# Optimization experiments

Measured on AMD Instinct MI355X. Metric: run time of the kernel, lower is better.

The kernel has to match this reference:

```python
import jax, jax.numpy as jnp
import numpy as np

DIM = 1024
DEPTH = 8
DIM_HEAD = 64
HEADS = 16
NUM_Q = 16
EMB = 768
OUT = 1024
FF_INNER = 4 * DIM
INNER = DIM_HEAD * HEADS  # 1024
B, N1 = 64, 577
EPS = 1e-5


def _ln(x, g, b):
    mu = jnp.mean(x, axis=-1, keepdims=True)
    var = jnp.mean((x - mu) ** 2, axis=-1, keepdims=True)
    return (x - mu) * jax.lax.rsqrt(var + EPS) * g + b


def setup_inputs() -> dict:
    key = jax.random.key(0)
    ks = jax.random.split(key, 16)
    std = 0.02
    inp = {
        'x': jax.random.normal(ks[0], (B, N1, EMB), jnp.float32),
        'queries': jax.random.normal(ks[1], (1, NUM_Q, DIM), jnp.float32) / DIM ** 0.5,
        'proj_in_w': jax.random.normal(ks[2], (EMB, DIM), jnp.float32) * std,
        'proj_in_b': jnp.zeros((DIM,), jnp.float32),
        'ln1_g': jnp.ones((DEPTH, DIM), jnp.float32),
        'ln1_b': jnp.zeros((DEPTH, DIM), jnp.float32),
        'ln2_g': jnp.ones((DEPTH, DIM), jnp.float32),
        'ln2_b': jnp.zeros((DEPTH, DIM), jnp.float32),
        'wq': jax.random.normal(ks[3], (DEPTH, DIM, INNER), jnp.float32) * std,
        'wkv': jax.random.normal(ks[4], (DEPTH, DIM, 2 * INNER), jnp.float32) * std,
        'wo': jax.random.normal(ks[5], (DEPTH, INNER, DIM), jnp.float32) * std,
        'ffln_g': jnp.ones((DEPTH, DIM), jnp.float32),
        'ffln_b': jnp.zeros((DEPTH, DIM), jnp.float32),
        'w1': jax.random.normal(ks[6], (DEPTH, DIM, FF_INNER), jnp.float32) * std,
        'w2': jax.random.normal(ks[7], (DEPTH, FF_INNER, DIM), jnp.float32) * std,
        'proj_out_w': jax.random.normal(ks[8], (DIM, OUT), jnp.float32) * std,
        'proj_out_b': jnp.zeros((OUT,), jnp.float32),
        'nout_g': jnp.ones((OUT,), jnp.float32),
        'nout_b': jnp.zeros((OUT,), jnp.float32),
    }
    return inp


def reference(x, queries, proj_in_w, proj_in_b, ln1_g, ln1_b, ln2_g, ln2_b,
              wq, wkv, wo, ffln_g, ffln_b, w1, w2,
              proj_out_w, proj_out_b, nout_g, nout_b):
    b = x.shape[0]
    xp = x @ proj_in_w + proj_in_b          # (b, n1, dim)
    latents0 = jnp.broadcast_to(queries, (b, NUM_Q, DIM))
    scale = DIM_HEAD ** -0.25               # applied to both q and k

    def layer(latents, p):
        (g1, b1, g2, b2, Wq, Wkv, Wo, gf, bf, W1, W2) = p
        xn = _ln(xp, g1, b1)                # (b, n1, dim)
        lt = _ln(latents, g2, b2)           # (b, nq, dim)
        q = lt @ Wq                         # (b, nq, inner)
        kv_in = jnp.concatenate([xn, lt], axis=1)   # (b, n1+nq, dim)
        kv = kv_in @ Wkv                    # (b, n1+nq, 2*inner)
        k, v = jnp.split(kv, 2, axis=-1)
        L = kv_in.shape[1]
        qh = q.reshape(b, NUM_Q, HEADS, DIM_HEAD).transpose(0, 2, 1, 3)
        kh = k.reshape(b, L, HEADS, DIM_HEAD).transpose(0, 2, 1, 3)
        vh = v.reshape(b, L, HEADS, DIM_HEAD).transpose(0, 2, 1, 3)
        logits = jnp.einsum('bhqd,bhkd->bhqk', qh * scale, kh * scale)
        w = jax.nn.softmax(logits.astype(jnp.float32), axis=-1).astype(logits.dtype)
        o = jnp.einsum('bhqk,bhkd->bhqd', w, vh)
        o = o.transpose(0, 2, 1, 3).reshape(b, NUM_Q, INNER) @ Wo
        latents = o + latents
        h = _ln(latents, gf, bf) @ W1
        h = jax.nn.gelu(h, approximate=False)
        latents = h @ W2 + latents
        return latents, None

    params = (ln1_g, ln1_b, ln2_g, ln2_b, wq, wkv, wo, ffln_g, ffln_b, w1, w2)
    latents, _ = jax.lax.scan(layer, latents0, params)
    out = latents @ proj_out_w + proj_out_b
    return _ln(out, nout_g, nout_b)
```

## Files before the change

kernel.cpp:

```cpp
#include <hip/hip_runtime.h>
#include <hip/hip_bf16.h>
#include <math.h>

#define DEV __device__ __forceinline__

typedef __bf16 bf16x8 __attribute__((ext_vector_type(8)));
typedef float f32x4 __attribute__((ext_vector_type(4)));
typedef unsigned short u16x8 __attribute__((ext_vector_type(8)));
typedef unsigned short u16x4 __attribute__((ext_vector_type(4)));

DEV float b2f(unsigned short u){ unsigned int i = ((unsigned int)u)<<16; float f; __builtin_memcpy(&f,&i,4); return f; }
DEV unsigned short f2b(float x){ unsigned int i; __builtin_memcpy(&i,&x,4); unsigned int r = i + 0x7FFFu + ((i>>16)&1u); return (unsigned short)(r>>16); }

DEV int swz(int row, int elem){ return row*64 + ((((elem>>3) ^ row) & 7)<<3) + (elem&7); }

enum { EPI_F32=0, EPI_GELU=2, EPI_RESF32=3 };

template<int BM, int BN>
__global__ __launch_bounds__(256)
void gemm_lds(const unsigned short* __restrict__ A, const unsigned short* __restrict__ Bt,
              const float* __restrict__ bias, unsigned short* __restrict__ Out,
              int M, int N, int K, int NT)
{
    constexpr int MR = BM/32, NR = BN/32;
    constexpr int SA = BM/8, SB = BN/8;
    __shared__ unsigned short As[BM*64];
    __shared__ unsigned short Bs[BN*64];
    const int tid  = threadIdx.x;
    const int lane = tid & 63;
    const int wave = tid >> 6;
    const int wr = wave >> 1, wc = wave & 1;
    const int chunk = gridDim.x >> 3;
    const int nb = (blockIdx.x & 7)*chunk + (blockIdx.x >> 3);
    const int nt = nb % NT, mt = nb / NT;
    const int lr = lane >> 3;
    const int lc = lane & 7;

    f32x4 acc[MR][NR];
    #pragma unroll
    for (int m=0;m<MR;m++)
      #pragma unroll
      for (int n=0;n<NR;n++) acc[m][n] = f32x4{0.f,0.f,0.f,0.f};

    auto stage = [&](int k0){
      #pragma unroll
      for (int i=0;i<SA/4;i++){
        int s = wave*(SA/4) + i;
        int row = s*8 + lr;
        const unsigned short* src = A + (size_t)(mt*BM+row)*K + k0 + (((lc ^ row)&7)<<3);
        __builtin_amdgcn_global_load_lds((const unsigned int*)src, (unsigned int*)&As[s*512], 16, 0, 0);
      }
      #pragma unroll
      for (int i=0;i<SB/4;i++){
        int s = wave*(SB/4) + i;
        int row = s*8 + lr;
        const unsigned short* src = Bt + (size_t)(nt*BN+row)*K + k0 + (((lc ^ row)&7)<<3);
        __builtin_amdgcn_global_load_lds((const unsigned int*)src, (unsigned int*)&Bs[s*512], 16, 0, 0);
      }
    };

    const int nk = K / 64;
    #pragma unroll 1
    for (int kt=0; kt<nk; kt++){
      stage(kt*64);
      __syncthreads();
      #pragma unroll
      for (int kk=0; kk<2; kk++){
        bf16x8 av[MR], bv[NR];
        #pragma unroll
        for (int m=0;m<MR;m++){
          int r = wr*(BM/2) + m*16 + (lane&15);
          av[m] = (bf16x8)(*reinterpret_cast<const u16x8*>(&As[swz(r, kk*32 + (lane>>4)*8)]));
        }
        #pragma unroll
        for (int n=0;n<NR;n++){
          int r = wc*(BN/2) + n*16 + (lane&15);
          bv[n] = (bf16x8)(*reinterpret_cast<const u16x8*>(&Bs[swz(r, kk*32 + (lane>>4)*8)]));
        }
        #pragma unroll
        for (int m=0;m<MR;m++)
          #pragma unroll
          for (int n=0;n<NR;n++)
            acc[m][n] = __builtin_amdgcn_mfma_f32_16x16x32_bf16(av[m], bv[n], acc[m][n], 0, 0, 0);
      }
      __syncthreads();
    }

    #pragma unroll
    for (int m=0;m<MR;m++){
      #pragma unroll
      for (int n=0;n<NR;n++){
        #pragma unroll
        for (int r=0;r<4;r++){
          int row = mt*BM + wr*(BM/2) + m*16 + (lane>>4)*4 + r;
          int col = nt*BN + wc*(BN/2) + n*16 + (lane&15);
          if (row < M){
            float v = acc[m][n][r];
            if (bias) v += bias[col];
            Out[(size_t)row*N + col] = f2b(v);
          }
        }
      }
    }
}

template<int EPI>
__global__ __launch_bounds__(256)
void gemm_sp(const unsigned short* __restrict__ AH, const unsigned short* __restrict__ AL,
             const unsigned short* __restrict__ BH, const unsigned short* __restrict__ BL,
             const float* __restrict__ bias, const float* __restrict__ Res,
             void* __restrict__ Out, unsigned short* __restrict__ OutL,
             int M, int N, int K, int NT)
{
    constexpr int MR=2, NR=2;
    __shared__ unsigned short As[2*64*64];
    __shared__ unsigned short Bs[2*64*64];
    const int tid  = threadIdx.x;
    const int lane = tid & 63;
    const int wave = tid >> 6;
    const int wr = wave >> 1, wc = wave & 1;
    const int chunk = gridDim.x >> 3;
    const int nb = (blockIdx.x & 7)*chunk + (blockIdx.x >> 3);
    const int nt = nb % NT, mt = nb / NT;
    const int lr = lane >> 3;
    const int lc = lane & 7;

    f32x4 acc[MR][NR];
    #pragma unroll
    for (int m=0;m<MR;m++)
      #pragma unroll
      for (int n=0;n<NR;n++) acc[m][n] = f32x4{0.f,0.f,0.f,0.f};

    auto stage = [&](int k0){
      #pragma unroll
      for (int i=0;i<2;i++){
        int s = wave*2 + i;
        int row = s*8 + lr;
        int scol = ((lc ^ row)&7)<<3;
        size_t aofs = (size_t)(mt*64+row)*K + k0 + scol;
        size_t bofs = (size_t)(nt*64+row)*K + k0 + scol;
        __builtin_amdgcn_global_load_lds((const unsigned int*)(AH+aofs), (unsigned int*)&As[s*512],        16, 0, 0);
        __builtin_amdgcn_global_load_lds((const unsigned int*)(AL+aofs), (unsigned int*)&As[4096 + s*512], 16, 0, 0);
        __builtin_amdgcn_global_load_lds((const unsigned int*)(BH+bofs), (unsigned int*)&Bs[s*512],        16, 0, 0);
        __builtin_amdgcn_global_load_lds((const unsigned int*)(BL+bofs), (unsigned int*)&Bs[4096 + s*512], 16, 0, 0);
      }
    };

    const int nk = K / 64;
    #pragma unroll 1
    for (int kt=0; kt<nk; kt++){
      stage(kt*64);
      __syncthreads();
      #pragma unroll
      for (int kk=0; kk<2; kk++){
        bf16x8 ah[MR], al[MR], bh[NR], bl[NR];
        #pragma unroll
        for (int m=0;m<MR;m++){
          int a = swz(wr*32 + m*16 + (lane&15), kk*32 + (lane>>4)*8);
          ah[m] = (bf16x8)(*reinterpret_cast<const u16x8*>(&As[a]));
          al[m] = (bf16x8)(*reinterpret_cast<const u16x8*>(&As[4096 + a]));
        }
        #pragma unroll
        for (int n=0;n<NR;n++){
          int a = swz(wc*32 + n*16 + (lane&15), kk*32 + (lane>>4)*8);
          bh[n] = (bf16x8)(*reinterpret_cast<const u16x8*>(&Bs[a]));
          bl[n] = (bf16x8)(*reinterpret_cast<const u16x8*>(&Bs[4096 + a]));
        }
        #pragma unroll
        for (int m=0;m<MR;m++)
          #pragma unroll
          for (int n=0;n<NR;n++){
            acc[m][n] = __builtin_amdgcn_mfma_f32_16x16x32_bf16(ah[m], bh[n], acc[m][n], 0, 0, 0);
            acc[m][n] = __builtin_amdgcn_mfma_f32_16x16x32_bf16(ah[m], bl[n], acc[m][n], 0, 0, 0);
            acc[m][n] = __builtin_amdgcn_mfma_f32_16x16x32_bf16(al[m], bh[n], acc[m][n], 0, 0, 0);
          }
      }
      __syncthreads();
    }

    #pragma unroll
    for (int m=0;m<MR;m++){
      #pragma unroll
      for (int n=0;n<NR;n++){
        #pragma unroll
        for (int r=0;r<4;r++){
          int row = mt*64 + wr*32 + m*16 + (lane>>4)*4 + r;
          int col = nt*64 + wc*32 + n*16 + (lane&15);
          float v = acc[m][n][r];
          if (bias) v += bias[col];
          if constexpr (EPI==EPI_GELU){
            v = 0.5f*v*(1.0f + erff(v*0.70710678118654752f));
            unsigned short hi = f2b(v);
            ((unsigned short*)Out)[(size_t)row*N + col] = hi;
            OutL[(size_t)row*N + col] = f2b(v - b2f(hi));
          } else {
            if constexpr (EPI==EPI_RESF32) v += Res[(size_t)row*N + col];
            ((float*)Out)[(size_t)row*N + col] = v;
          }
        }
      }
    }
}

enum { OM_F32=0, OM_BF16=1, OM_SPLIT=2 };
template<bool INF32, int OM, bool HASGB>
__global__ __launch_bounds__(256)
void ln_rows(const void* __restrict__ In, void* __restrict__ Out,
             unsigned short* __restrict__ OutL,
             const float* __restrict__ g, const float* __restrict__ bb)
{
  const int row = blockIdx.x;
  const int tid = threadIdx.x;
  const size_t base = (size_t)row*1024 + tid*4;
  float v[4];
  if constexpr (INF32){
    f32x4 t = *reinterpret_cast<const f32x4*>((const float*)In + base);
    v[0]=t[0]; v[1]=t[1]; v[2]=t[2]; v[3]=t[3];
  } else {
    u16x4 t = *reinterpret_cast<const u16x4*>((const unsigned short*)In + base);
    #pragma unroll
    for (int j=0;j<4;j++) v[j] = b2f(t[j]);
  }
  float s = v[0]+v[1]+v[2]+v[3];
  float q = v[0]*v[0]+v[1]*v[1]+v[2]*v[2]+v[3]*v[3];
  #pragma unroll
  for (int o=32;o>0;o>>=1){ s += __shfl_xor(s,o,64); q += __shfl_xor(q,o,64); }
  __shared__ float sm[8];
  const int wave = tid>>6, lane = tid&63;
  if (lane==0){ sm[wave] = s; sm[4+wave] = q; }
  __syncthreads();
  s = sm[0]+sm[1]+sm[2]+sm[3];
  q = sm[4]+sm[5]+sm[6]+sm[7];
  const float mean = s*(1.f/1024.f);
  const float rstd = rsqrtf(fmaxf(q*(1.f/1024.f) - mean*mean, 0.f) + 1e-5f);
  #pragma unroll
  for (int j=0;j<4;j++){
    float t2 = (v[j]-mean)*rstd;
    if constexpr (HASGB) t2 = t2*g[tid*4+j] + bb[tid*4+j];
    v[j] = t2;
  }
  if constexpr (OM==OM_F32){
    f32x4 t{v[0],v[1],v[2],v[3]};
    *reinterpret_cast<f32x4*>((float*)Out + base) = t;
  } else if constexpr (OM==OM_BF16){
    u16x4 t{f2b(v[0]),f2b(v[1]),f2b(v[2]),f2b(v[3])};
    *reinterpret_cast<u16x4*>((unsigned short*)Out + base) = t;
  } else {
    u16x4 h{f2b(v[0]),f2b(v[1]),f2b(v[2]),f2b(v[3])};
    u16x4 l{f2b(v[0]-b2f(h[0])),f2b(v[1]-b2f(h[1])),f2b(v[2]-b2f(h[2])),f2b(v[3]-b2f(h[3]))};
    *reinterpret_cast<u16x4*>((unsigned short*)Out + base) = h;
    *reinterpret_cast<u16x4*>(OutL + base) = l;
  }
}

template<bool LO>
__global__ __launch_bounds__(256)
void transpose_cvt(const float* __restrict__ W, const float* __restrict__ rs,
                   unsigned short* __restrict__ Wt, unsigned short* __restrict__ Wtlo,
                   int K, int N)
{
  __shared__ float t[32][33];
  const int tx = threadIdx.x & 31, ty = threadIdx.x >> 5;
  const int n0 = blockIdx.x*32, k0 = blockIdx.y*32;
  #pragma unroll
  for (int j=0;j<4;j++){
    int r = ty + j*8;
    float w = W[(size_t)(k0+r)*N + n0 + tx];
    if (rs) w *= rs[k0+r];
    t[r][tx] = w;
  }
  __syncthreads();
  #pragma unroll
  for (int j=0;j<4;j++){
    int r = ty + j*8;
    float w = t[tx][r];
    unsigned short hi = f2b(w);
    Wt[(size_t)(n0+r)*K + k0 + tx] = hi;
    if constexpr (LO)
      Wtlo[(size_t)(n0+r)*K + k0 + tx] = f2b(w - b2f(hi));
  }
}

__global__ __launch_bounds__(256)
void biaskv_kernel(const float* __restrict__ ln1b, const float* __restrict__ wkv,
                   float* __restrict__ out)
{
  const int l = blockIdx.y;
  const int n = blockIdx.x*256 + threadIdx.x;
  const float* b1 = ln1b + l*1024;
  const float* W  = wkv + (size_t)l*1024*2048;
  float s = 0.f;
  for (int k=0;k<1024;k++) s += b1[k]*W[(size_t)k*2048 + n];
  out[l*2048 + n] = s;
}

__global__ __launch_bounds__(256)
void init_latents(const float* __restrict__ Q, float* __restrict__ L)
{
  size_t idx = ((size_t)blockIdx.x*256 + threadIdx.x)*4;
  int row = (int)(idx >> 10);
  int col = (int)(idx & 1023);
  f32x4 t = *reinterpret_cast<const f32x4*>(Q + (size_t)(row & 15)*1024 + col);
  *reinterpret_cast<f32x4*>(L + idx) = t;
}

__global__ __launch_bounds__(256)
void cvt_f32_bf16(const float* __restrict__ In, unsigned short* __restrict__ Out, size_t n4)
{
  size_t i = (size_t)blockIdx.x*256 + threadIdx.x;
  if (i >= n4) return;
  f32x4 t = *reinterpret_cast<const f32x4*>(In + i*4);
  u16x4 u{f2b(t[0]),f2b(t[1]),f2b(t[2]),f2b(t[3])};
  *reinterpret_cast<u16x4*>(Out + i*4) = u;
}

__global__ __launch_bounds__(256)
void cvt_f32b_pair(const float* __restrict__ In, unsigned short* __restrict__ Oh,
                   unsigned short* __restrict__ Ol)
{
  size_t idx = ((size_t)blockIdx.x*256 + threadIdx.x)*4;
  f32x4 t = *reinterpret_cast<const f32x4*>(In + idx);
  u16x4 h{f2b(t[0]),f2b(t[1]),f2b(t[2]),f2b(t[3])};
  u16x4 l{f2b(t[0]-b2f(h[0])),f2b(t[1]-b2f(h[1])),f2b(t[2]-b2f(h[2])),f2b(t[3]-b2f(h[3]))};
  *reinterpret_cast<u16x4*>(Oh + idx) = h;
  *reinterpret_cast<u16x4*>(Ol + idx) = l;
}

__global__ __launch_bounds__(256)
void attn_kernel(const float* __restrict__ QLTf,
                 const unsigned short* __restrict__ KVX,
                 const float* __restrict__ KVLTf,
                 unsigned short* __restrict__ ATTOh,
                 unsigned short* __restrict__ ATTOl)
{
  __shared__ float qs[16][64];
  __shared__ float ws[16][600];
  const int tid = threadIdx.x;
  const int bh = blockIdx.x;
  const int b = bh >> 4, h = bh & 15;

  {
    int idx = tid*4;
    int qi = idx >> 6, d = idx & 63;
    f32x4 t = *reinterpret_cast<const f32x4*>(QLTf + (size_t)(b*16+qi)*1024 + h*64 + d);
    #pragma unroll
    for (int j=0;j<4;j++) qs[qi][d+j] = 0.125f * t[j];
  }
  __syncthreads();

  for (int r = tid; r < 593; r += 256){
    float a[16];
    #pragma unroll
    for (int qi=0;qi<16;qi++) a[qi] = 0.f;
    if (r < 577){
      const unsigned short* krow = KVX + ((size_t)(b*577 + r)*2048 + h*64);
      #pragma unroll 4
      for (int d4=0; d4<16; d4++){
        u16x4 k4 = *reinterpret_cast<const u16x4*>(krow + d4*4);
        float kf0=b2f(k4[0]), kf1=b2f(k4[1]), kf2=b2f(k4[2]), kf3=b2f(k4[3]);
        #pragma unroll
        for (int qi=0;qi<16;qi++){
          f32x4 q4 = *reinterpret_cast<const f32x4*>(&qs[qi][d4*4]);
          a[qi] += q4[0]*kf0 + q4[1]*kf1 + q4[2]*kf2 + q4[3]*kf3;
        }
      }
    } else {
      const float* krow = KVLTf + ((size_t)(b*16 + (r-577))*2048 + h*64);
      #pragma unroll 4
      for (int d4=0; d4<16; d4++){
        f32x4 k4 = *reinterpret_cast<const f32x4*>(krow + d4*4);
        #pragma unroll
        for (int qi=0;qi<16;qi++){
          f32x4 q4 = *reinterpret_cast<const f32x4*>(&qs[qi][d4*4]);
          a[qi] += q4[0]*k4[0] + q4[1]*k4[1] + q4[2]*k4[2] + q4[3]*k4[3];
        }
      }
    }
    #pragma unroll
    for (int qi=0;qi<16;qi++) ws[qi][r] = a[qi];
  }
  __syncthreads();

  const int wave = tid>>6, lane = tid&63;
  for (int qi = wave; qi < 16; qi += 4){
    float m = -1e30f;
    for (int r = lane; r < 593; r += 64) m = fmaxf(m, ws[qi][r]);
    #pragma unroll
    for (int o=32;o>0;o>>=1) m = fmaxf(m, __shfl_xor(m,o,64));
    float s = 0.f;
    for (int r = lane; r < 593; r += 64){ float e = expf(ws[qi][r]-m); ws[qi][r] = e; s += e; }
    #pragma unroll
    for (int o=32;o>0;o>>=1) s += __shfl_xor(s,o,64);
    float inv = 1.f/s;
    for (int r = lane; r < 593; r += 64) ws[qi][r] *= inv;
  }
  __syncthreads();

  const int d = tid & 63, qg = tid >> 6;
  float o0=0.f,o1=0.f,o2=0.f,o3=0.f;
  for (int rr=0; rr<576; rr+=4){
    f32x4 w0 = *reinterpret_cast<const f32x4*>(&ws[qg   ][rr]);
    f32x4 w1 = *reinterpret_cast<const f32x4*>(&ws[qg+4 ][rr]);
    f32x4 w2 = *reinterpret_cast<const f32x4*>(&ws[qg+8 ][rr]);
    f32x4 w3 = *reinterpret_cast<const f32x4*>(&ws[qg+12][rr]);
    #pragma unroll
    for (int j=0;j<4;j++){
      const unsigned short* vrow = KVX + ((size_t)(b*577 + rr + j)*2048 + 1024 + h*64);
      float v = b2f(vrow[d]);
      o0 += w0[j]*v; o1 += w1[j]*v; o2 += w2[j]*v; o3 += w3[j]*v;
    }
  }
  {
    float v = b2f(KVX[(size_t)(b*577 + 576)*2048 + 1024 + h*64 + d]);
    o0 += ws[qg][576]*v; o1 += ws[qg+4][576]*v; o2 += ws[qg+8][576]*v; o3 += ws[qg+12][576]*v;
  }
  for (int r=577; r<593; r++){
    float v = KVLTf[(size_t)(b*16 + (r-577))*2048 + 1024 + h*64 + d];
    o0 += ws[qg][r]*v; o1 += ws[qg+4][r]*v; o2 += ws[qg+8][r]*v; o3 += ws[qg+12][r]*v;
  }
  float ov[4] = {o0,o1,o2,o3};
  #pragma unroll
  for (int j=0;j<4;j++){
    size_t idx = (size_t)(b*16+qg+4*j)*1024 + h*64 + d;
    unsigned short hi = f2b(ov[j]);
    ATTOh[idx] = hi;
    ATTOl[idx] = f2b(ov[j] - b2f(hi));
  }
}

extern "C" void kernel_launch(void* const* d_in, const int* in_sizes, int n_in,
                              void* d_out, int out_size, void* d_ws, size_t ws_size,
                              hipStream_t stream)
{
  const float* x    = (const float*)d_in[0];
  const float* qry  = (const float*)d_in[1];
  const float* piw  = (const float*)d_in[2];
  const float* pib  = (const float*)d_in[3];
  const float* ln1g = (const float*)d_in[4];
  const float* ln1b = (const float*)d_in[5];
  const float* ln2g = (const float*)d_in[6];
  const float* ln2b = (const float*)d_in[7];
  const float* wq   = (const float*)d_in[8];
  const float* wkv  = (const float*)d_in[9];
  const float* wo   = (const float*)d_in[10];
  const float* ffg  = (const float*)d_in[11];
  const float* ffb  = (const float*)d_in[12];
  const float* w1   = (const float*)d_in[13];
  const float* w2   = (const float*)d_in[14];
  const float* pow_ = (const float*)d_in[15];
  const float* pob  = (const float*)d_in[16];
  const float* ng   = (const float*)d_in[17];
  const float* nb   = (const float*)d_in[18];

  const int MROWS = 64*577;
  char* wsb = (char*)d_ws;
  size_t off = 0;
  auto alloc = [&](size_t bytes)->char*{
    char* p = wsb + off; off = (off + bytes + 255) & ~(size_t)255; return p;
  };
  unsigned short* XB    = (unsigned short*)alloc((size_t)36992*768*2);
  unsigned short* XP    = (unsigned short*)alloc((size_t)36992*1024*2);
  unsigned short* KVX   = (unsigned short*)alloc((size_t)36992*2048*2);
  unsigned short* WpiT  = (unsigned short*)alloc((size_t)1024*768*2);
  unsigned short* WkvTs = (unsigned short*)alloc((size_t)2048*1024*2);
  unsigned short* WkvT  = (unsigned short*)alloc((size_t)2048*1024*2);
  unsigned short* WkvTl = (unsigned short*)alloc((size_t)2048*1024*2);
  unsigned short* WqT   = (unsigned short*)alloc((size_t)1024*1024*2);
  unsigned short* WqTl  = (unsigned short*)alloc((size_t)1024*1024*2);
  unsigned short* WoT   = (unsigned short*)alloc((size_t)1024*1024*2);
  unsigned short* WoTl  = (unsigned short*)alloc((size_t)1024*1024*2);
  unsigned short* W1T   = (unsigned short*)alloc((size_t)4096*1024*2);
  unsigned short* W1Tl  = (unsigned short*)alloc((size_t)4096*1024*2);
  unsigned short* W2T   = (unsigned short*)alloc((size_t)1024*4096*2);
  unsigned short* W2Tl  = (unsigned short*)alloc((size_t)1024*4096*2);
  float*          BKV   = (float*)alloc((size_t)8*2048*4);
  unsigned short* LTh   = (unsigned short*)alloc((size_t)1024*1024*2);
  unsigned short* LTl   = (unsigned short*)alloc((size_t)1024*1024*2);
  float*          QLTf  = (float*)alloc((size_t)1024*1024*4);
  float*          KVLTf = (float*)alloc((size_t)1024*2048*4);
  unsigned short* ATTOh = (unsigned short*)alloc((size_t)1024*1024*2);
  unsigned short* ATTOl = (unsigned short*)alloc((size_t)1024*1024*2);
  unsigned short* FFHh  = (unsigned short*)alloc((size_t)1024*4096*2);
  unsigned short* FFHl  = (unsigned short*)alloc((size_t)1024*4096*2);
  unsigned short* LATBh = (unsigned short*)alloc((size_t)1024*1024*2);
  unsigned short* LATBl = (unsigned short*)alloc((size_t)1024*1024*2);
  float*          LATF  = (float*)alloc((size_t)1024*1024*4);
  if (off > ws_size) return;

  dim3 blk(256);

  cvt_f32_bf16<<<dim3((36928*768/4 + 255)/256), blk, 0, stream>>>(x, XB, (size_t)36928*768/4);
  transpose_cvt<false><<<dim3(32,24), blk, 0, stream>>>(piw, nullptr, WpiT, nullptr, 768, 1024);
  biaskv_kernel<<<dim3(8,8),   blk, 0, stream>>>(ln1b, wkv, BKV);
  init_latents<<<dim3(1024),   blk, 0, stream>>>(qry, LATF);

  gemm_lds<128,128><<<dim3(8*289), blk, 0, stream>>>(
      XB, WpiT, pib, XP, MROWS, 1024, 768, 8);
  ln_rows<false,OM_BF16,false><<<dim3(MROWS), blk, 0, stream>>>(XP, XP, nullptr, nullptr, nullptr);

  for (int l=0; l<8; l++){
    transpose_cvt<false><<<dim3(64,32),  blk, 0, stream>>>(wkv + (size_t)l*1024*2048, ln1g + l*1024, WkvTs, nullptr, 1024, 2048);
    transpose_cvt<true ><<<dim3(64,32),  blk, 0, stream>>>(wkv + (size_t)l*1024*2048, nullptr, WkvT, WkvTl, 1024, 2048);
    transpose_cvt<true ><<<dim3(32,32),  blk, 0, stream>>>(wq  + (size_t)l*1024*1024, nullptr, WqT,  WqTl, 1024, 1024);
    transpose_cvt<true ><<<dim3(32,32),  blk, 0, stream>>>(wo  + (size_t)l*1024*1024, nullptr, WoT,  WoTl, 1024, 1024);
    transpose_cvt<true ><<<dim3(128,32), blk, 0, stream>>>(w1  + (size_t)l*1024*4096, nullptr, W1T,  W1Tl, 1024, 4096);
    transpose_cvt<true ><<<dim3(32,128), blk, 0, stream>>>(w2  + (size_t)l*4096*1024, nullptr, W2T,  W2Tl, 4096, 1024);

    ln_rows<true,OM_SPLIT,true><<<dim3(1024), blk, 0, stream>>>(LATF, LTh, LTl, ln2g + l*1024, ln2b + l*1024);
    gemm_sp<EPI_F32><<<dim3(16*16), blk, 0, stream>>>(
        LTh, LTl, WqT, WqTl, nullptr, nullptr, QLTf, nullptr, 1024, 1024, 1024, 16);
    gemm_sp<EPI_F32><<<dim3(16*32), blk, 0, stream>>>(
        LTh, LTl, WkvT, WkvTl, nullptr, nullptr, KVLTf, nullptr, 1024, 2048, 1024, 32);
    gemm_lds<128,128><<<dim3(16*289), blk, 0, stream>>>(
        XP, WkvTs, BKV + l*2048, KVX, MROWS, 2048, 1024, 16);
    attn_kernel<<<dim3(1024), blk, 0, stream>>>(QLTf, KVX, KVLTf, ATTOh, ATTOl);
    gemm_sp<EPI_RESF32><<<dim3(16*16), blk, 0, stream>>>(
        ATTOh, ATTOl, WoT, WoTl, nullptr, LATF, LATF, nullptr, 1024, 1024, 1024, 16);
    ln_rows<true,OM_SPLIT,true><<<dim3(1024), blk, 0, stream>>>(LATF, LTh, LTl, ffg + l*1024, ffb + l*1024);
    gemm_sp<EPI_GELU><<<dim3(16*64), blk, 0, stream>>>(
        LTh, LTl, W1T, W1Tl, nullptr, nullptr, FFHh, FFHl, 1024, 4096, 1024, 64);
    gemm_sp<EPI_RESF32><<<dim3(16*16), blk, 0, stream>>>(
        FFHh, FFHl, W2T, W2Tl, nullptr, LATF, LATF, nullptr, 1024, 1024, 4096, 16);
  }

  transpose_cvt<true><<<dim3(32,32), blk, 0, stream>>>(pow_, nullptr, WqT, WqTl, 1024, 1024);
  cvt_f32b_pair<<<dim3(1024), blk, 0, stream>>>(LATF, LATBh, LATBl);
  gemm_sp<EPI_F32><<<dim3(16*16), blk, 0, stream>>>(
      LATBh, LATBl, WqT, WqTl, pob, nullptr, QLTf, nullptr, 1024, 1024, 1024, 16);
  ln_rows<true,OM_F32,true><<<dim3(1024), blk, 0, stream>>>(QLTf, d_out, nullptr, ng, nb);
}
```

Baseline: 6.099 ms.

## Double-buffer GEMM LDS staging, fuse Q/KV latent GEMMs, batch weight transposes

Both GEMM kernels now double-buffer their LDS tiles. The next K-tile load is issued right after a single barrier, so memory traffic overlaps MFMA work, and row pointers are precomputed with clamped A rows. The separate Q and KV projections of the latents are merged into one GEMM over a concatenated 3072-wide weight, and the attention kernel reads from that combined buffer. The per-layer transposes of Wq, Wkv and Wo are hoisted into batched launches over all 8 layers before the loop, which costs more workspace and doubles LDS per block.

New measurement: 5.926 ms. 2.8% less time.

```diff
diff --git a/kernel.cpp b/kernel.cpp
--- a/kernel.cpp
+++ b/kernel.cpp
@@ -18,14 +18,14 @@
 
 template<int BM, int BN>
 __global__ __launch_bounds__(256)
-void gemm_lds(const unsigned short* __restrict__ A, const unsigned short* __restrict__ Bt,
-              const float* __restrict__ bias, unsigned short* __restrict__ Out,
-              int M, int N, int K, int NT)
+void gemm2(const unsigned short* __restrict__ A, const unsigned short* __restrict__ Bt,
+           const float* __restrict__ bias, unsigned short* __restrict__ Out,
+           int M, int N, int K, int NT)
 {
     constexpr int MR = BM/32, NR = BN/32;
-    constexpr int SA = BM/8, SB = BN/8;
-    __shared__ unsigned short As[BM*64];
-    __shared__ unsigned short Bs[BN*64];
+    constexpr int LA = BM/32, LB = BN/32;
+    __shared__ unsigned short As[2][BM*64];
+    __shared__ unsigned short Bs[2][BN*64];
     const int tid  = threadIdx.x;
     const int lane = tid & 63;
     const int wave = tid >> 6;
@@ -42,40 +42,54 @@
       #pragma unroll
       for (int n=0;n<NR;n++) acc[m][n] = f32x4{0.f,0.f,0.f,0.f};
 
-    auto stage = [&](int k0){
-      #pragma unroll
-      for (int i=0;i<SA/4;i++){
-        int s = wave*(SA/4) + i;
-        int row = s*8 + lr;
-        const unsigned short* src = A + (size_t)(mt*BM+row)*K + k0 + (((lc ^ row)&7)<<3);
-        __builtin_amdgcn_global_load_lds((const unsigned int*)src, (unsigned int*)&As[s*512], 16, 0, 0);
-      }
-      #pragma unroll
-      for (int i=0;i<SB/4;i++){
-        int s = wave*(SB/4) + i;
-        int row = s*8 + lr;
-        const unsigned short* src = Bt + (size_t)(nt*BN+row)*K + k0 + (((lc ^ row)&7)<<3);
-        __builtin_amdgcn_global_load_lds((const unsigned int*)src, (unsigned int*)&Bs[s*512], 16, 0, 0);
+    const unsigned short* pA[LA];
+    const unsigned short* pB[LB];
+    #pragma unroll
+    for (int i=0;i<LA;i++){
+      int s = wave*LA + i; int row = s*8 + lr;
+      int gr = mt*BM + row; if (gr > M-1) gr = M-1;
+      pA[i] = A + (size_t)gr*K + (((lc ^ row)&7)<<3);
+    }
+    #pragma unroll
+    for (int i=0;i<LB;i++){
+      int s = wave*LB + i; int row = s*8 + lr;
+      pB[i] = Bt + (size_t)(nt*BN+row)*K + (((lc ^ row)&7)<<3);
+    }
+
+    auto stage = [&](int buf, int k0){
+      #pragma unroll
+      for (int i=0;i<LA;i++){
+        int s = wave*LA + i;
+        __builtin_amdgcn_global_load_lds((const unsigned int*)(pA[i]+k0), (unsigned int*)&As[buf][s*512], 16, 0, 0);
+      }
+      #pragma unroll
+      for (int i=0;i<LB;i++){
+        int s = wave*LB + i;
+        __builtin_amdgcn_global_load_lds((const unsigned int*)(pB[i]+k0), (unsigned int*)&Bs[buf][s*512], 16, 0, 0);
       }
     };
 
+    stage(0, 0);
     const int nk = K / 64;
     #pragma unroll 1
     for (int kt=0; kt<nk; kt++){
-      stage(kt*64);
-      __syncthreads();
+      const int cur = kt & 1;
+      asm volatile("s_waitcnt vmcnt(0)" ::: "memory");
+      __builtin_amdgcn_s_barrier();
+      __builtin_amdgcn_sched_barrier(0);
+      if (kt+1 < nk) stage(cur^1, (kt+1)*64);
       #pragma unroll
       for (int kk=0; kk<2; kk++){
         bf16x8 av[MR], bv[NR];
         #pragma unroll
         for (int m=0;m<MR;m++){
           int r = wr*(BM/2) + m*16 + (lane&15);
-          av[m] = (bf16x8)(*reinterpret_cast<const u16x8*>(&As[swz(r, kk*32 + (lane>>4)*8)]));
+          av[m] = (bf16x8)(*reinterpret_cast<const u16x8*>(&As[cur][swz(r, kk*32 + (lane>>4)*8)]));
         }
         #pragma unroll
         for (int n=0;n<NR;n++){
           int r = wc*(BN/2) + n*16 + (lane&15);
-          bv[n] = (bf16x8)(*reinterpret_cast<const u16x8*>(&Bs[swz(r, kk*32 + (lane>>4)*8)]));
+          bv[n] = (bf16x8)(*reinterpret_cast<const u16x8*>(&Bs[cur][swz(r, kk*32 + (lane>>4)*8)]));
         }
         #pragma unroll
         for (int m=0;m<MR;m++)
@@ -83,7 +97,6 @@
           for (int n=0;n<NR;n++)
             acc[m][n] = __builtin_amdgcn_mfma_f32_16x16x32_bf16(av[m], bv[n], acc[m][n], 0, 0, 0);
       }
-      __syncthreads();
     }
 
     #pragma unroll
@@ -106,15 +119,15 @@
 
 template<int EPI>
 __global__ __launch_bounds__(256)
-void gemm_sp(const unsigned short* __restrict__ AH, const unsigned short* __restrict__ AL,
-             const unsigned short* __restrict__ BH, const unsigned short* __restrict__ BL,
-             const float* __restrict__ bias, const float* __restrict__ Res,
-             void* __restrict__ Out, unsigned short* __restrict__ OutL,
-             int M, int N, int K, int NT)
+void gemm_sp2(const unsigned short* __restrict__ AH, const unsigned short* __restrict__ AL,
+              const unsigned short* __restrict__ BH, const unsigned short* __restrict__ BL,
+              const float* __restrict__ bias, const float* __restrict__ Res,
+              void* __restrict__ Out, unsigned short* __restrict__ OutL,
+              int M, int N, int K, int NT)
 {
     constexpr int MR=2, NR=2;
-    __shared__ unsigned short As[2*64*64];
-    __shared__ unsigned short Bs[2*64*64];
+    __shared__ unsigned short As[2][2][64*64];
+    __shared__ unsigned short Bs[2][2][64*64];
     const int tid  = threadIdx.x;
     const int lane = tid & 63;
     const int wave = tid >> 6;
@@ -131,40 +144,50 @@
       #pragma unroll
       for (int n=0;n<NR;n++) acc[m][n] = f32x4{0.f,0.f,0.f,0.f};
 
-    auto stage = [&](int k0){
+    const unsigned short *pAH[2], *pAL[2], *pBH[2], *pBL[2];
+    #pragma unroll
+    for (int i=0;i<2;i++){
+      int s = wave*2 + i; int row = s*8 + lr; int scol = ((lc ^ row)&7)<<3;
+      size_t aofs = (size_t)(mt*64+row)*K + scol;
+      size_t bofs = (size_t)(nt*64+row)*K + scol;
+      pAH[i] = AH + aofs; pAL[i] = AL + aofs;
+      pBH[i] = BH + bofs; pBL[i] = BL + bofs;
+    }
+
+    auto stage = [&](int buf, int k0){
       #pragma unroll
       for (int i=0;i<2;i++){
         int s = wave*2 + i;
-        int row = s*8 + lr;
-        int scol = ((lc ^ row)&7)<<3;
-        size_t aofs = (size_t)(mt*64+row)*K + k0 + scol;
-        size_t bofs = (size_t)(nt*64+row)*K + k0 + scol;
-        __builtin_amdgcn_global_load_lds((const unsigned int*)(AH+aofs), (unsigned int*)&As[s*512],        16, 0, 0);
-        __builtin_amdgcn_global_load_lds((const unsigned int*)(AL+aofs), (unsigned int*)&As[4096 + s*512], 16, 0, 0);
-        __builtin_amdgcn_global_load_lds((const unsigned int*)(BH+bofs), (unsigned int*)&Bs[s*512],        16, 0, 0);
-        __builtin_amdgcn_global_load_lds((const unsigned int*)(BL+bofs), (unsigned int*)&Bs[4096 + s*512], 16, 0, 0);
+        __builtin_amdgcn_global_load_lds((const unsigned int*)(pAH[i]+k0), (unsigned int*)&As[buf][0][s*512], 16, 0, 0);
+        __builtin_amdgcn_global_load_lds((const unsigned int*)(pAL[i]+k0), (unsigned int*)&As[buf][1][s*512], 16, 0, 0);
+        __builtin_amdgcn_global_load_lds((const unsigned int*)(pBH[i]+k0), (unsigned int*)&Bs[buf][0][s*512], 16, 0, 0);
+        __builtin_amdgcn_global_load_lds((const unsigned int*)(pBL[i]+k0), (unsigned int*)&Bs[buf][1][s*512], 16, 0, 0);
       }
     };
 
+    stage(0, 0);
     const int nk = K / 64;
     #pragma unroll 1
     for (int kt=0; kt<nk; kt++){
-      stage(kt*64);
-      __syncthreads();
+      const int cur = kt & 1;
+      asm volatile("s_waitcnt vmcnt(0)" ::: "memory");
+      __builtin_amdgcn_s_barrier();
+      __builtin_amdgcn_sched_barrier(0);
+      if (kt+1 < nk) stage(cur^1, (kt+1)*64);
       #pragma unroll
       for (int kk=0; kk<2; kk++){
         bf16x8 ah[MR], al[MR], bh[NR], bl[NR];
         #pragma unroll
         for (int m=0;m<MR;m++){
           int a = swz(wr*32 + m*16 + (lane&15), kk*32 + (lane>>4)*8);
-          ah[m] = (bf16x8)(*reinterpret_cast<const u16x8*>(&As[a]));
-          al[m] = (bf16x8)(*reinterpret_cast<const u16x8*>(&As[4096 + a]));
+          ah[m] = (bf16x8)(*reinterpret_cast<const u16x8*>(&As[cur][0][a]));
+          al[m] = (bf16x8)(*reinterpret_cast<const u16x8*>(&As[cur][1][a]));
         }
         #pragma unroll
         for (int n=0;n<NR;n++){
           int a = swz(wc*32 + n*16 + (lane&15), kk*32 + (lane>>4)*8);
-          bh[n] = (bf16x8)(*reinterpret_cast<const u16x8*>(&Bs[a]));
-          bl[n] = (bf16x8)(*reinterpret_cast<const u16x8*>(&Bs[4096 + a]));
+          bh[n] = (bf16x8)(*reinterpret_cast<const u16x8*>(&Bs[cur][0][a]));
+          bl[n] = (bf16x8)(*reinterpret_cast<const u16x8*>(&Bs[cur][1][a]));
         }
         #pragma unroll
         for (int m=0;m<MR;m++)
@@ -175,7 +198,6 @@
             acc[m][n] = __builtin_amdgcn_mfma_f32_16x16x32_bf16(al[m], bh[n], acc[m][n], 0, 0, 0);
           }
       }
-      __syncthreads();
     }
 
     #pragma unroll
@@ -255,18 +277,20 @@
 
 template<bool LO>
 __global__ __launch_bounds__(256)
-void transpose_cvt(const float* __restrict__ W, const float* __restrict__ rs,
-                   unsigned short* __restrict__ Wt, unsigned short* __restrict__ Wtlo,
-                   int K, int N)
-{
+void transpose_cvt_b(const float* __restrict__ W, const float* __restrict__ rs,
+                     unsigned short* __restrict__ Wt, unsigned short* __restrict__ Wtlo,
+                     int K, int N, size_t wLS, size_t tLS, int dstRowOff)
+{
+  const int l = blockIdx.z;
+  const float* Wl = W + (size_t)l*wLS;
   __shared__ float t[32][33];
   const int tx = threadIdx.x & 31, ty = threadIdx.x >> 5;
   const int n0 = blockIdx.x*32, k0 = blockIdx.y*32;
   #pragma unroll
   for (int j=0;j<4;j++){
     int r = ty + j*8;
-    float w = W[(size_t)(k0+r)*N + n0 + tx];
-    if (rs) w *= rs[k0+r];
+    float w = Wl[(size_t)(k0+r)*N + n0 + tx];
+    if (rs) w *= rs[l*1024 + k0+r];
     t[r][tx] = w;
   }
   __syncthreads();
@@ -275,9 +299,9 @@
     int r = ty + j*8;
     float w = t[tx][r];
     unsigned short hi = f2b(w);
-    Wt[(size_t)(n0+r)*K + k0 + tx] = hi;
-    if constexpr (LO)
-      Wtlo[(size_t)(n0+r)*K + k0 + tx] = f2b(w - b2f(hi));
+    size_t di = (size_t)l*tLS + (size_t)(dstRowOff + n0 + r)*K + k0 + tx;
+    Wt[di] = hi;
+    if constexpr (LO) Wtlo[di] = f2b(w - b2f(hi));
   }
 }
 
@@ -327,9 +351,8 @@
 }
 
 __global__ __launch_bounds__(256)
-void attn_kernel(const float* __restrict__ QLTf,
+void attn_kernel(const float* __restrict__ QKVf,
                  const unsigned short* __restrict__ KVX,
-                 const float* __restrict__ KVLTf,
                  unsigned short* __restrict__ ATTOh,
                  unsigned short* __restrict__ ATTOl)
 {
@@ -342,7 +365,7 @@
   {
     int idx = tid*4;
     int qi = idx >> 6, d = idx & 63;
-    f32x4 t = *reinterpret_cast<const f32x4*>(QLTf + (size_t)(b*16+qi)*1024 + h*64 + d);
+    f32x4 t = *reinterpret_cast<const f32x4*>(QKVf + (size_t)(b*16+qi)*3072 + h*64 + d);
     #pragma unroll
     for (int j=0;j<4;j++) qs[qi][d+j] = 0.125f * t[j];
   }
@@ -365,7 +388,7 @@
         }
       }
     } else {
-      const float* krow = KVLTf + ((size_t)(b*16 + (r-577))*2048 + h*64);
+      const float* krow = QKVf + (size_t)(b*16 + (r-577))*3072 + 1024 + h*64;
       #pragma unroll 4
       for (int d4=0; d4<16; d4++){
         f32x4 k4 = *reinterpret_cast<const f32x4*>(krow + d4*4);
@@ -415,7 +438,7 @@
     o0 += ws[qg][576]*v; o1 += ws[qg+4][576]*v; o2 += ws[qg+8][576]*v; o3 += ws[qg+12][576]*v;
   }
   for (int r=577; r<593; r++){
-    float v = KVLTf[(size_t)(b*16 + (r-577))*2048 + 1024 + h*64 + d];
+    float v = QKVf[(size_t)(b*16 + (r-577))*3072 + 2048 + h*64 + d];
     o0 += ws[qg][r]*v; o1 += ws[qg+4][r]*v; o2 += ws[qg+8][r]*v; o3 += ws[qg+12][r]*v;
   }
   float ov[4] = {o0,o1,o2,o3};
@@ -458,74 +481,70 @@
   auto alloc = [&](size_t bytes)->char*{
     char* p = wsb + off; off = (off + bytes + 255) & ~(size_t)255; return p;
   };
-  unsigned short* XB    = (unsigned short*)alloc((size_t)36992*768*2);
-  unsigned short* XP    = (unsigned short*)alloc((size_t)36992*1024*2);
-  unsigned short* KVX   = (unsigned short*)alloc((size_t)36992*2048*2);
-  unsigned short* WpiT  = (unsigned short*)alloc((size_t)1024*768*2);
-  unsigned short* WkvTs = (unsigned short*)alloc((size_t)2048*1024*2);
-  unsigned short* WkvT  = (unsigned short*)alloc((size_t)2048*1024*2);
-  unsigned short* WkvTl = (unsigned short*)alloc((size_t)2048*1024*2);
-  unsigned short* WqT   = (unsigned short*)alloc((size_t)1024*1024*2);
-  unsigned short* WqTl  = (unsigned short*)alloc((size_t)1024*1024*2);
-  unsigned short* WoT   = (unsigned short*)alloc((size_t)1024*1024*2);
-  unsigned short* WoTl  = (unsigned short*)alloc((size_t)1024*1024*2);
-  unsigned short* W1T   = (unsigned short*)alloc((size_t)4096*1024*2);
-  unsigned short* W1Tl  = (unsigned short*)alloc((size_t)4096*1024*2);
-  unsigned short* W2T   = (unsigned short*)alloc((size_t)1024*4096*2);
-  unsigned short* W2Tl  = (unsigned short*)alloc((size_t)1024*4096*2);
-  float*          BKV   = (float*)alloc((size_t)8*2048*4);
-  unsigned short* LTh   = (unsigned short*)alloc((size_t)1024*1024*2);
-  unsigned short* LTl   = (unsigned short*)alloc((size_t)1024*1024*2);
-  float*          QLTf  = (float*)alloc((size_t)1024*1024*4);
-  float*          KVLTf = (float*)alloc((size_t)1024*2048*4);
-  unsigned short* ATTOh = (unsigned short*)alloc((size_t)1024*1024*2);
-  unsigned short* ATTOl = (unsigned short*)alloc((size_t)1024*1024*2);
-  unsigned short* FFHh  = (unsigned short*)alloc((size_t)1024*4096*2);
-  unsigned short* FFHl  = (unsigned short*)alloc((size_t)1024*4096*2);
-  unsigned short* LATBh = (unsigned short*)alloc((size_t)1024*1024*2);
-  unsigned short* LATBl = (unsigned short*)alloc((size_t)1024*1024*2);
-  float*          LATF  = (float*)alloc((size_t)1024*1024*4);
+  unsigned short* XB     = (unsigned short*)alloc((size_t)36992*768*2);
+  unsigned short* XP     = (unsigned short*)alloc((size_t)36992*1024*2);
+  unsigned short* KVX    = (unsigned short*)alloc((size_t)36992*2048*2);
+  unsigned short* WpiT   = (unsigned short*)alloc((size_t)1024*768*2);
+  unsigned short* WkvTs  = (unsigned short*)alloc((size_t)8*2048*1024*2);
+  unsigned short* WqkvT  = (unsigned short*)alloc((size_t)8*3072*1024*2);
+  unsigned short* WqkvTl = (unsigned short*)alloc((size_t)8*3072*1024*2);
+  unsigned short* WoT    = (unsigned short*)alloc((size_t)8*1024*1024*2);
+  unsigned short* WoTl   = (unsigned short*)alloc((size_t)8*1024*1024*2);
+  unsigned short* W1T    = (unsigned short*)alloc((size_t)4096*1024*2);
+  unsigned short* W1Tl   = (unsigned short*)alloc((size_t)4096*1024*2);
+  unsigned short* W2T    = (unsigned short*)alloc((size_t)1024*4096*2);
+  unsigned short* W2Tl   = (unsigned short*)alloc((size_t)1024*4096*2);
+  float*          BKV    = (float*)alloc((size_t)8*2048*4);
+  unsigned short* LTh    = (unsigned short*)alloc((size_t)1024*1024*2);
+  unsigned short* LTl    = (unsigned short*)alloc((size_t)1024*1024*2);
+  float*          QKVf   = (float*)alloc((size_t)1024*3072*4);
+  unsigned short* ATTOh  = (unsigned short*)alloc((size_t)1024*1024*2);
+  unsigned short* ATTOl  = (unsigned short*)alloc((size_t)1024*1024*2);
+  unsigned short* FFHh   = (unsigned short*)alloc((size_t)1024*4096*2);
+  unsigned short* FFHl   = (unsigned short*)alloc((size_t)1024*4096*2);
+  unsigned short* LATBh  = (unsigned short*)alloc((size_t)1024*1024*2);
+  unsigned short* LATBl  = (unsigned short*)alloc((size_t)1024*1024*2);
+  float*          LATF   = (float*)alloc((size_t)1024*1024*4);
   if (off > ws_size) return;
 
   dim3 blk(256);
 
   cvt_f32_bf16<<<dim3((36928*768/4 + 255)/256), blk, 0, stream>>>(x, XB, (size_t)36928*768/4);
-  transpose_cvt<false><<<dim3(32,24), blk, 0, stream>>>(piw, nullptr, WpiT, nullptr, 768, 1024);
-  biaskv_kernel<<<dim3(8,8),   blk, 0, stream>>>(ln1b, wkv, BKV);
-  init_latents<<<dim3(1024),   blk, 0, stream>>>(qry, LATF);
-
-  gemm_lds<128,128><<<dim3(8*289), blk, 0, stream>>>(
-      XB, WpiT, pib, XP, MROWS, 1024, 768, 8);
+  transpose_cvt_b<false><<<dim3(32,24,1), blk, 0, stream>>>(piw, nullptr, WpiT, nullptr, 768, 1024, 0, 0, 0);
+  transpose_cvt_b<false><<<dim3(64,32,8), blk, 0, stream>>>(wkv, ln1g, WkvTs, nullptr, 1024, 2048, (size_t)1024*2048, (size_t)2048*1024, 0);
+  transpose_cvt_b<true ><<<dim3(32,32,8), blk, 0, stream>>>(wq,  nullptr, WqkvT, WqkvTl, 1024, 1024, (size_t)1024*1024, (size_t)3072*1024, 0);
+  transpose_cvt_b<true ><<<dim3(64,32,8), blk, 0, stream>>>(wkv, nullptr, WqkvT, WqkvTl, 1024, 2048, (size_t)1024*2048, (size_t)3072*1024, 1024);
+  transpose_cvt_b<true ><<<dim3(32,32,8), blk, 0, stream>>>(wo,  nullptr, WoT, WoTl, 1024, 1024, (size_t)1024*1024, (size_t)1024*1024, 0);
+  biaskv_kernel<<<dim3(8,8), blk, 0, stream>>>(ln1b, wkv, BKV);
+  init_latents<<<dim3(1024), blk, 0, stream>>>(qry, LATF);
+
+  gemm2<128,128><<<dim3(8*289), blk, 0, stream>>>(XB, WpiT, pib, XP, MROWS, 1024, 768, 8);
   ln_rows<false,OM_BF16,false><<<dim3(MROWS), blk, 0, stream>>>(XP, XP, nullptr, nullptr, nullptr);
 
   for (int l=0; l<8; l++){
-    transpose_cvt<false><<<dim3(64,32),  blk, 0, stream>>>(wkv + (size_t)l*1024*2048, ln1g + l*1024, WkvTs, nullptr, 1024, 2048);
-    transpose_cvt<true ><<<dim3(64,32),  blk, 0, stream>>>(wkv + (size_t)l*1024*2048, nullptr, WkvT, WkvTl, 1024, 2048);
-    transpose_cvt<true ><<<dim3(32,32),  blk, 0, stream>>>(wq  + (size_t)l*1024*1024, nullptr, WqT,  WqTl, 1024, 1024);
-    transpose_cvt<true ><<<dim3(32,32),  blk, 0, stream>>>(wo  + (size_t)l*1024*1024, nullptr, WoT,  WoTl, 1024, 1024);
-    transpose_cvt<true ><<<dim3(128,32), blk, 0, stream>>>(w1  + (size_t)l*1024*4096, nullptr, W1T,  W1Tl, 1024, 4096);
-    transpose_cvt<true ><<<dim3(32,128), blk, 0, stream>>>(w2  + (size_t)l*4096*1024, nullptr, W2T,  W2Tl, 4096, 1024);
+    transpose_cvt_b<true><<<dim3(128,32,1), blk, 0, stream>>>(w1 + (size_t)l*1024*4096, nullptr, W1T, W1Tl, 1024, 4096, 0, 0, 0);
+    transpose_cvt_b<true><<<dim3(32,128,1), blk, 0, stream>>>(w2 + (size_t)l*4096*1024, nullptr, W2T, W2Tl, 4096, 1024, 0, 0, 0);
 
     ln_rows<true,OM_SPLIT,true><<<dim3(1024), blk, 0, stream>>>(LATF, LTh, LTl, ln2g + l*1024, ln2b + l*1024);
-    gemm_sp<EPI_F32><<<dim3(16*16), blk, 0, stream>>>(
-        LTh, LTl, WqT, WqTl, nullptr, nullptr, QLTf, nullptr, 1024, 1024, 1024, 16);
-    gemm_sp<EPI_F32><<<dim3(16*32), blk, 0, stream>>>(
-        LTh, LTl, WkvT, WkvTl, nullptr, nullptr, KVLTf, nullptr, 1024, 2048, 1024, 32);
-    gemm_lds<128,128><<<dim3(16*289), blk, 0, stream>>>(
-        XP, WkvTs, BKV + l*2048, KVX, MROWS, 2048, 1024, 16);
-    attn_kernel<<<dim3(1024), blk, 0, stream>>>(QLTf, KVX, KVLTf, ATTOh, ATTOl);
-    gemm_sp<EPI_RESF32><<<dim3(16*16), blk, 0, stream>>>(
-        ATTOh, ATTOl, WoT, WoTl, nullptr, LATF, LATF, nullptr, 1024, 1024, 1024, 16);
+    gemm_sp2<EPI_F32><<<dim3(16*48), blk, 0, stream>>>(
+        LTh, LTl, WqkvT + (size_t)l*3072*1024, WqkvTl + (size_t)l*3072*1024,
+        nullptr, nullptr, QKVf, nullptr, 1024, 3072, 1024, 48);
+    gemm2<128,128><<<dim3(16*289), blk, 0, stream>>>(
+        XP, WkvTs + (size_t)l*2048*1024, BKV + l*2048, KVX, MROWS, 2048, 1024, 16);
+    attn_kernel<<<dim3(1024), blk, 0, stream>>>(QKVf, KVX, ATTOh, ATTOl);
+    gemm_sp2<EPI_RESF32><<<dim3(16*16), blk, 0, stream>>>(
+        ATTOh, ATTOl, WoT + (size_t)l*1024*1024, WoTl + (size_t)l*1024*1024,
+        nullptr, LATF, LATF, nullptr, 1024, 1024, 1024, 16);
     ln_rows<true,OM_SPLIT,true><<<dim3(1024), blk, 0, stream>>>(LATF, LTh, LTl, ffg + l*1024, ffb + l*1024);
-    gemm_sp<EPI_GELU><<<dim3(16*64), blk, 0, stream>>>(
+    gemm_sp2<EPI_GELU><<<dim3(16*64), blk, 0, stream>>>(
         LTh, LTl, W1T, W1Tl, nullptr, nullptr, FFHh, FFHl, 1024, 4096, 1024, 64);
-    gemm_sp<EPI_RESF32><<<dim3(16*16), blk, 0, stream>>>(
+    gemm_sp2<EPI_RESF32><<<dim3(16*16), blk, 0, stream>>>(
         FFHh, FFHl, W2T, W2Tl, nullptr, LATF, LATF, nullptr, 1024, 1024, 4096, 16);
   }
 
-  transpose_cvt<true><<<dim3(32,32), blk, 0, stream>>>(pow_, nullptr, WqT, WqTl, 1024, 1024);
+  transpose_cvt_b<true><<<dim3(32,32,1), blk, 0, stream>>>(pow_, nullptr, W1T, W1Tl, 1024, 1024, 0, 0, 0);
   cvt_f32b_pair<<<dim3(1024), blk, 0, stream>>>(LATF, LATBh, LATBl);
-  gemm_sp<EPI_F32><<<dim3(16*16), blk, 0, stream>>>(
-      LATBh, LATBl, WqT, WqTl, pob, nullptr, QLTf, nullptr, 1024, 1024, 1024, 16);
-  ln_rows<true,OM_F32,true><<<dim3(1024), blk, 0, stream>>>(QLTf, d_out, nullptr, ng, nb);
-}
+  gemm_sp2<EPI_F32><<<dim3(16*16), blk, 0, stream>>>(
+      LATBh, LATBl, W1T, W1Tl, pob, nullptr, QKVf, nullptr, 1024, 1024, 1024, 16);
+  ln_rows<true,OM_F32,true><<<dim3(1024), blk, 0, stream>>>(QKVf, d_out, nullptr, ng, nb);
+}
```
